# Kernel tuning notes

Hardware: AMD Instinct MI355X
Metric: run time of the kernel (lower is better)

The kernel has to match this reference:

```python
import jax, jax.numpy as jnp
import numpy as np
from jax.scipy.linalg import expm as _expm

B, D = 1024, 128
_SQRT3 = 3.0 ** 0.5
_C1, _C2 = 0.5 - _SQRT3 / 6.0, 0.5 + _SQRT3 / 6.0


def setup_inputs() -> dict:
    key = jax.random.key(0)
    k_t, k_y, k_a, k_w = jax.random.split(key, 4)
    scale = 1.0 / np.sqrt(D)  # keep ||Omega|| moderate so expm is well-conditioned
    return {
        "t0": jax.random.uniform(k_t, (B,), dtype=jnp.float32),
        "h": jnp.float32(0.1),
        "y0": jax.random.normal(k_y, (B, D), dtype=jnp.float32),
        "A0": jax.random.normal(k_a, (B, D, D), dtype=jnp.float32) * scale,
        "W": jax.random.normal(k_w, (B, D, D), dtype=jnp.float32) * scale,
    }


def reference(t0, h, y0, A0, W):
    # A(t) = A0 + t * W evaluated at the two Gauss-Legendre nodes
    t1 = t0 + _C1 * h  # (B,)
    t2 = t0 + _C2 * h  # (B,)
    A1 = A0 + t1[:, None, None] * W  # (B, D, D)
    A2 = A0 + t2[:, None, None] * W  # (B, D, D)
    alpha1 = (h * 0.5) * (A1 + A2)
    alpha2 = (h * _SQRT3) * (A2 - A1)
    comm = alpha1 @ alpha2 - alpha2 @ alpha1  # [alpha1, alpha2]
    Omega = alpha1 - comm / 12.0
    U = jax.vmap(_expm)(Omega)  # batched matrix exponential (B, D, D)
    y_next = jnp.einsum("bij,bj->bi", U, y0)  # (B, D)
    return y_next, jnp.stack((A1, A2), axis=0)
```

## Files before the change

### kernel.cpp

```cpp
#include <hip/hip_runtime.h>

#define B_SZ 1024
#define D_SZ 128
#define KTERMS 8
#define RSTRIDE 68

typedef float vfloat4 __attribute__((ext_vector_type(4)));

__device__ inline float bflo(unsigned u) { return __uint_as_float(u << 16); }
__device__ inline float bfhi(unsigned u) { return __uint_as_float(u & 0xffff0000u); }

__device__ inline float dotlds(const unsigned* rq, const float* v) {
    float a0 = 0.f, a1 = 0.f, a2 = 0.f, a3 = 0.f;
#pragma unroll
    for (int j = 0; j < 8; ++j) {
        uint4 qq = *(const uint4*)(rq + 4 * j);
        vfloat4 v0 = *(const vfloat4*)(v + 8 * j);
        vfloat4 v1 = *(const vfloat4*)(v + 8 * j + 4);
        a0 = fmaf(bflo(qq.x), v0.x, a0);
        a1 = fmaf(bfhi(qq.x), v0.y, a1);
        a2 = fmaf(bflo(qq.y), v0.z, a2);
        a3 = fmaf(bfhi(qq.y), v0.w, a3);
        a0 = fmaf(bflo(qq.z), v1.x, a0);
        a1 = fmaf(bfhi(qq.z), v1.y, a1);
        a2 = fmaf(bflo(qq.w), v1.z, a2);
        a3 = fmaf(bfhi(qq.w), v1.w, a3);
    }
    return (a0 + a1) + (a2 + a3);
}

__global__ void __launch_bounds__(512, 4)
magnus_kernel(const float* __restrict__ t0p, const float* __restrict__ hp,
              const float* __restrict__ y0, const float* __restrict__ A0,
              const float* __restrict__ W, float* __restrict__ out)
{
    __shared__ __align__(16) unsigned sA[D_SZ * RSTRIDE];
    __shared__ __align__(16) unsigned sW[D_SZ * RSTRIDE];
    __shared__ __align__(16) float sv[D_SZ];
    __shared__ __align__(16) float su1[D_SZ];
    __shared__ __align__(16) float su2[D_SZ];
    __shared__ __align__(16) float su3[D_SZ];
    __shared__ __align__(16) float su4[D_SZ];

    const int b = blockIdx.x;
    const int tid = threadIdx.x;
    const float h = hp[0];
    const float tb = t0p[b];
    const float SQ3_6 = 0.28867513459481287f;
    const float t1 = tb + (0.5f - SQ3_6) * h;
    const float t2 = tb + (0.5f + SQ3_6) * h;

    const size_t moff = (size_t)b * (D_SZ * D_SZ);
    const float4* A0v = (const float4*)(A0 + moff);
    const float4* Wv  = (const float4*)(W + moff);
    vfloat4* o1 = (vfloat4*)(out + (size_t)B_SZ * D_SZ + moff);
    vfloat4* o2 = (vfloat4*)(out + (size_t)B_SZ * D_SZ
                                 + (size_t)B_SZ * D_SZ * D_SZ + moff);

#pragma unroll 8
    for (int it = 0; it < 8; ++it) {
        int i = it * 512 + tid;
        float4 a = A0v[i];
        float4 w = Wv[i];
        vfloat4 p1, p2;
        p1.x = fmaf(t1, w.x, a.x); p1.y = fmaf(t1, w.y, a.y);
        p1.z = fmaf(t1, w.z, a.z); p1.w = fmaf(t1, w.w, a.w);
        p2.x = fmaf(t2, w.x, a.x); p2.y = fmaf(t2, w.y, a.y);
        p2.z = fmaf(t2, w.z, a.z); p2.w = fmaf(t2, w.w, a.w);
        __builtin_nontemporal_store(p1, o1 + i);
        __builtin_nontemporal_store(p2, o2 + i);

        unsigned pa0, pa1, pw0, pw1;
        asm("v_cvt_pk_bf16_f32 %0, %1, %2" : "=v"(pa0) : "v"(a.x), "v"(a.y));
        asm("v_cvt_pk_bf16_f32 %0, %1, %2" : "=v"(pa1) : "v"(a.z), "v"(a.w));
        asm("v_cvt_pk_bf16_f32 %0, %1, %2" : "=v"(pw0) : "v"(w.x), "v"(w.y));
        asm("v_cvt_pk_bf16_f32 %0, %1, %2" : "=v"(pw1) : "v"(w.z), "v"(w.w));
        int r = i >> 5;
        int p = (2 * i) & 63;
        *(uint2*)(&sA[r * RSTRIDE + p]) = make_uint2(pa0, pa1);
        *(uint2*)(&sW[r * RSTRIDE + p]) = make_uint2(pw0, pw1);
    }

    const int grp  = tid >> 8;
    const int t8   = tid & 255;
    const int half = (t8 >> 5) & 1;
    const int row  = (t8 & 31) + ((t8 >> 6) << 5);
    const unsigned* rq = (grp ? sW : sA) + row * RSTRIDE + half * 32;

    float yacc = 0.0f;
    if (tid < D_SZ) {
        float v = y0[(size_t)b * D_SZ + tid];
        sv[tid] = v;
        yacc = v;
    }
    __syncthreads();

    const float hs = h * (tb + 0.5f * h);
    const float c3 = h * h * h * (1.0f / 12.0f);

#pragma unroll
    for (int k = 1; k <= KTERMS; ++k) {
        float a = dotlds(rq, sv + half * 64);
        a += __shfl_xor(a, 32);
        if (!half) { if (grp == 0) su1[row] = a; else su2[row] = a; }
        __syncthreads();
        const float* vb = grp ? su1 : su2;
        float c = dotlds(rq, vb + half * 64);
        c += __shfl_xor(c, 32);
        if (!half) { if (grp == 0) su3[row] = c; else su4[row] = c; }
        __syncthreads();
        if (tid < D_SZ) {
            float wn = h * su1[tid] + hs * su2[tid] - c3 * (su3[tid] - su4[tid]);
            wn *= (1.0f / (float)k);
            yacc += wn;
            sv[tid] = wn;
        }
        __syncthreads();
    }

    if (tid < D_SZ) {
        out[(size_t)b * D_SZ + tid] = yacc;
    }
}

extern "C" void kernel_launch(void* const* d_in, const int* in_sizes, int n_in,
                              void* d_out, int out_size, void* d_ws, size_t ws_size,
                              hipStream_t stream) {
    const float* t0 = (const float*)d_in[0];
    const float* h  = (const float*)d_in[1];
    const float* y0 = (const float*)d_in[2];
    const float* A0 = (const float*)d_in[3];
    const float* W  = (const float*)d_in[4];
    float* out = (float*)d_out;
    magnus_kernel<<<B_SZ, 512, 0, stream>>>(t0, h, y0, A0, W, out);
}
```

Measured before the change: 257.2 us.

## Process two batches per block and prefetch next matrices into registers

```diff
diff --git a/kernel.cpp b/kernel.cpp
--- a/kernel.cpp
+++ b/kernel.cpp
@@ -4,6 +4,7 @@
 #define D_SZ 128
 #define KTERMS 8
 #define RSTRIDE 68
+#define NBATCH 2
 
 typedef float vfloat4 __attribute__((ext_vector_type(4)));
 
@@ -42,44 +43,9 @@
     __shared__ __align__(16) float su3[D_SZ];
     __shared__ __align__(16) float su4[D_SZ];
 
-    const int b = blockIdx.x;
     const int tid = threadIdx.x;
     const float h = hp[0];
-    const float tb = t0p[b];
     const float SQ3_6 = 0.28867513459481287f;
-    const float t1 = tb + (0.5f - SQ3_6) * h;
-    const float t2 = tb + (0.5f + SQ3_6) * h;
-
-    const size_t moff = (size_t)b * (D_SZ * D_SZ);
-    const float4* A0v = (const float4*)(A0 + moff);
-    const float4* Wv  = (const float4*)(W + moff);
-    vfloat4* o1 = (vfloat4*)(out + (size_t)B_SZ * D_SZ + moff);
-    vfloat4* o2 = (vfloat4*)(out + (size_t)B_SZ * D_SZ
-                                 + (size_t)B_SZ * D_SZ * D_SZ + moff);
-
-#pragma unroll 8
-    for (int it = 0; it < 8; ++it) {
-        int i = it * 512 + tid;
-        float4 a = A0v[i];
-        float4 w = Wv[i];
-        vfloat4 p1, p2;
-        p1.x = fmaf(t1, w.x, a.x); p1.y = fmaf(t1, w.y, a.y);
-        p1.z = fmaf(t1, w.z, a.z); p1.w = fmaf(t1, w.w, a.w);
-        p2.x = fmaf(t2, w.x, a.x); p2.y = fmaf(t2, w.y, a.y);
-        p2.z = fmaf(t2, w.z, a.z); p2.w = fmaf(t2, w.w, a.w);
-        __builtin_nontemporal_store(p1, o1 + i);
-        __builtin_nontemporal_store(p2, o2 + i);
-
-        unsigned pa0, pa1, pw0, pw1;
-        asm("v_cvt_pk_bf16_f32 %0, %1, %2" : "=v"(pa0) : "v"(a.x), "v"(a.y));
-        asm("v_cvt_pk_bf16_f32 %0, %1, %2" : "=v"(pa1) : "v"(a.z), "v"(a.w));
-        asm("v_cvt_pk_bf16_f32 %0, %1, %2" : "=v"(pw0) : "v"(w.x), "v"(w.y));
-        asm("v_cvt_pk_bf16_f32 %0, %1, %2" : "=v"(pw1) : "v"(w.z), "v"(w.w));
-        int r = i >> 5;
-        int p = (2 * i) & 63;
-        *(uint2*)(&sA[r * RSTRIDE + p]) = make_uint2(pa0, pa1);
-        *(uint2*)(&sW[r * RSTRIDE + p]) = make_uint2(pw0, pw1);
-    }
 
     const int grp  = tid >> 8;
     const int t8   = tid & 255;
@@ -87,39 +53,102 @@
     const int row  = (t8 & 31) + ((t8 >> 6) << 5);
     const unsigned* rq = (grp ? sW : sA) + row * RSTRIDE + half * 32;
 
-    float yacc = 0.0f;
-    if (tid < D_SZ) {
-        float v = y0[(size_t)b * D_SZ + tid];
-        sv[tid] = v;
-        yacc = v;
+    int b = blockIdx.x * NBATCH;
+
+    vfloat4 ra[8], rw[8];
+    {
+        const vfloat4* A0n = (const vfloat4*)(A0 + (size_t)b * (D_SZ * D_SZ));
+        const vfloat4* Wn  = (const vfloat4*)(W  + (size_t)b * (D_SZ * D_SZ));
+#pragma unroll
+        for (int it = 0; it < 8; ++it) {
+            int i = it * 512 + tid;
+            ra[it] = A0n[i];
+            rw[it] = Wn[i];
+        }
     }
-    __syncthreads();
 
-    const float hs = h * (tb + 0.5f * h);
-    const float c3 = h * h * h * (1.0f / 12.0f);
+    for (int g = 0; g < NBATCH; ++g, ++b) {
+        const float tb = t0p[b];
+        const float t1 = tb + (0.5f - SQ3_6) * h;
+        const float t2 = tb + (0.5f + SQ3_6) * h;
+        const size_t moff = (size_t)b * (D_SZ * D_SZ);
+        vfloat4* o1 = (vfloat4*)(out + (size_t)B_SZ * D_SZ + moff);
+        vfloat4* o2 = (vfloat4*)(out + (size_t)B_SZ * D_SZ
+                                     + (size_t)B_SZ * D_SZ * D_SZ + moff);
 
 #pragma unroll
-    for (int k = 1; k <= KTERMS; ++k) {
-        float a = dotlds(rq, sv + half * 64);
-        a += __shfl_xor(a, 32);
-        if (!half) { if (grp == 0) su1[row] = a; else su2[row] = a; }
+        for (int it = 0; it < 8; ++it) {
+            int i = it * 512 + tid;
+            vfloat4 a = ra[it], w = rw[it];
+            vfloat4 p1, p2;
+            p1.x = fmaf(t1, w.x, a.x); p1.y = fmaf(t1, w.y, a.y);
+            p1.z = fmaf(t1, w.z, a.z); p1.w = fmaf(t1, w.w, a.w);
+            p2.x = fmaf(t2, w.x, a.x); p2.y = fmaf(t2, w.y, a.y);
+            p2.z = fmaf(t2, w.z, a.z); p2.w = fmaf(t2, w.w, a.w);
+            __builtin_nontemporal_store(p1, o1 + i);
+            __builtin_nontemporal_store(p2, o2 + i);
+
+            unsigned pa0, pa1, pw0, pw1;
+            asm("v_cvt_pk_bf16_f32 %0, %1, %2" : "=v"(pa0) : "v"(a.x), "v"(a.y));
+            asm("v_cvt_pk_bf16_f32 %0, %1, %2" : "=v"(pa1) : "v"(a.z), "v"(a.w));
+            asm("v_cvt_pk_bf16_f32 %0, %1, %2" : "=v"(pw0) : "v"(w.x), "v"(w.y));
+            asm("v_cvt_pk_bf16_f32 %0, %1, %2" : "=v"(pw1) : "v"(w.z), "v"(w.w));
+            int r = i >> 5;
+            int p = (2 * i) & 63;
+            *(uint2*)(&sA[r * RSTRIDE + p]) = make_uint2(pa0, pa1);
+            *(uint2*)(&sW[r * RSTRIDE + p]) = make_uint2(pw0, pw1);
+        }
+
+        float yacc = 0.0f;
+        if (tid < D_SZ) {
+            float v = y0[(size_t)b * D_SZ + tid];
+            sv[tid] = v;
+            yacc = v;
+        }
+
+        if (g + 1 < NBATCH) {
+            const vfloat4* A0n = (const vfloat4*)(A0 + moff + D_SZ * D_SZ);
+            const vfloat4* Wn  = (const vfloat4*)(W  + moff + D_SZ * D_SZ);
+#pragma unroll
+            for (int it = 0; it < 8; ++it) {
+                int i = it * 512 + tid;
+                ra[it] = A0n[i];
+                rw[it] = Wn[i];
+            }
+#pragma unroll
+            for (int it = 0; it < 8; ++it) {
+                asm volatile("" : "+v"(ra[it]));
+                asm volatile("" : "+v"(rw[it]));
+            }
+        }
+
         __syncthreads();
-        const float* vb = grp ? su1 : su2;
-        float c = dotlds(rq, vb + half * 64);
-        c += __shfl_xor(c, 32);
-        if (!half) { if (grp == 0) su3[row] = c; else su4[row] = c; }
-        __syncthreads();
+
+        const float hs = h * (tb + 0.5f * h);
+        const float c3 = h * h * h * (1.0f / 12.0f);
+#pragma unroll
+        for (int k = 1; k <= KTERMS; ++k) {
+            float a = dotlds(rq, sv + half * 64);
+            a += __shfl_xor(a, 32);
+            if (!half) { if (grp == 0) su1[row] = a; else su2[row] = a; }
+            __syncthreads();
+            const float* vb = grp ? su1 : su2;
+            float c = dotlds(rq, vb + half * 64);
+            c += __shfl_xor(c, 32);
+            if (!half) { if (grp == 0) su3[row] = c; else su4[row] = c; }
+            __syncthreads();
+            if (tid < D_SZ) {
+                float wn = h * su1[tid] + hs * su2[tid] - c3 * (su3[tid] - su4[tid]);
+                wn *= (1.0f / (float)k);
+                yacc += wn;
+                sv[tid] = wn;
+            }
+            __syncthreads();
+        }
+
         if (tid < D_SZ) {
-            float wn = h * su1[tid] + hs * su2[tid] - c3 * (su3[tid] - su4[tid]);
-            wn *= (1.0f / (float)k);
-            yacc += wn;
-            sv[tid] = wn;
+            out[(size_t)b * D_SZ + tid] = yacc;
         }
-        __syncthreads();
-    }
-
-    if (tid < D_SZ) {
-        out[(size_t)b * D_SZ + tid] = yacc;
     }
 }
 
@@ -132,5 +161,5 @@
     const float* A0 = (const float*)d_in[3];
     const float* W  = (const float*)d_in[4];
     float* out = (float*)d_out;
-    magnus_kernel<<<B_SZ, 512, 0, stream>>>(t0, h, y0, A0, W, out);
+    magnus_kernel<<<B_SZ / NBATCH, 512, 0, stream>>>(t0, h, y0, A0, W, out);
 }
```

After: 269.5 us. 4.8% more time.

## Keep bf16 A0/W rows in registers instead of LDS and cut Taylor terms to 7

Applied to the files above, without the earlier changes.

```diff
diff --git a/kernel.cpp b/kernel.cpp
--- a/kernel.cpp
+++ b/kernel.cpp
@@ -2,29 +2,23 @@
 
 #define B_SZ 1024
 #define D_SZ 128
-#define KTERMS 8
-#define RSTRIDE 68
+#define KTERMS 7
+#define QPAD 36
 
 typedef float vfloat4 __attribute__((ext_vector_type(4)));
 
 __device__ inline float bflo(unsigned u) { return __uint_as_float(u << 16); }
 __device__ inline float bfhi(unsigned u) { return __uint_as_float(u & 0xffff0000u); }
 
-__device__ inline float dotlds(const unsigned* rq, const float* v) {
+__device__ inline float dot32(const unsigned* rq, const float* v) {
     float a0 = 0.f, a1 = 0.f, a2 = 0.f, a3 = 0.f;
 #pragma unroll
     for (int j = 0; j < 8; ++j) {
-        uint4 qq = *(const uint4*)(rq + 4 * j);
-        vfloat4 v0 = *(const vfloat4*)(v + 8 * j);
-        vfloat4 v1 = *(const vfloat4*)(v + 8 * j + 4);
-        a0 = fmaf(bflo(qq.x), v0.x, a0);
-        a1 = fmaf(bfhi(qq.x), v0.y, a1);
-        a2 = fmaf(bflo(qq.y), v0.z, a2);
-        a3 = fmaf(bfhi(qq.y), v0.w, a3);
-        a0 = fmaf(bflo(qq.z), v1.x, a0);
-        a1 = fmaf(bfhi(qq.z), v1.y, a1);
-        a2 = fmaf(bflo(qq.w), v1.z, a2);
-        a3 = fmaf(bfhi(qq.w), v1.w, a3);
+        vfloat4 vv = *(const vfloat4*)(v + 4 * j);
+        a0 = fmaf(bflo(rq[2 * j]),     vv.x, a0);
+        a1 = fmaf(bfhi(rq[2 * j]),     vv.y, a1);
+        a2 = fmaf(bflo(rq[2 * j + 1]), vv.z, a2);
+        a3 = fmaf(bfhi(rq[2 * j + 1]), vv.w, a3);
     }
     return (a0 + a1) + (a2 + a3);
 }
@@ -34,86 +28,85 @@
               const float* __restrict__ y0, const float* __restrict__ A0,
               const float* __restrict__ W, float* __restrict__ out)
 {
-    __shared__ __align__(16) unsigned sA[D_SZ * RSTRIDE];
-    __shared__ __align__(16) unsigned sW[D_SZ * RSTRIDE];
-    __shared__ __align__(16) float sv[D_SZ];
-    __shared__ __align__(16) float su1[D_SZ];
-    __shared__ __align__(16) float su2[D_SZ];
-    __shared__ __align__(16) float su3[D_SZ];
-    __shared__ __align__(16) float su4[D_SZ];
+    __shared__ __align__(16) float svr [4 * QPAD];
+    __shared__ __align__(16) float su1r[4 * QPAD];
+    __shared__ __align__(16) float su2r[4 * QPAD];
+    __shared__ __align__(16) float su3r[4 * QPAD];
+    __shared__ __align__(16) float su4r[4 * QPAD];
 
-    const int b = blockIdx.x;
+    const int b   = blockIdx.x;
     const int tid = threadIdx.x;
-    const float h = hp[0];
+    const int row = tid >> 2;
+    const int q   = tid & 3;
+    const float h  = hp[0];
     const float tb = t0p[b];
     const float SQ3_6 = 0.28867513459481287f;
     const float t1 = tb + (0.5f - SQ3_6) * h;
     const float t2 = tb + (0.5f + SQ3_6) * h;
 
     const size_t moff = (size_t)b * (D_SZ * D_SZ);
-    const float4* A0v = (const float4*)(A0 + moff);
-    const float4* Wv  = (const float4*)(W + moff);
-    vfloat4* o1 = (vfloat4*)(out + (size_t)B_SZ * D_SZ + moff);
-    vfloat4* o2 = (vfloat4*)(out + (size_t)B_SZ * D_SZ
-                                 + (size_t)B_SZ * D_SZ * D_SZ + moff);
+    const int fbase = row * 32 + q * 8;
+    const float4* Ap = (const float4*)(A0 + moff) + fbase;
+    const float4* Wp = (const float4*)(W + moff) + fbase;
+    float4* o1 = (float4*)(out + (size_t)B_SZ * D_SZ + moff) + fbase;
+    float4* o2 = (float4*)(out + (size_t)B_SZ * D_SZ
+                               + (size_t)B_SZ * D_SZ * D_SZ + moff) + fbase;
 
-#pragma unroll 8
+    unsigned ra[16], rw[16];
+#pragma unroll
     for (int it = 0; it < 8; ++it) {
-        int i = it * 512 + tid;
-        float4 a = A0v[i];
-        float4 w = Wv[i];
-        vfloat4 p1, p2;
+        float4 a = Ap[it];
+        float4 w = Wp[it];
+        float4 p1, p2;
         p1.x = fmaf(t1, w.x, a.x); p1.y = fmaf(t1, w.y, a.y);
         p1.z = fmaf(t1, w.z, a.z); p1.w = fmaf(t1, w.w, a.w);
         p2.x = fmaf(t2, w.x, a.x); p2.y = fmaf(t2, w.y, a.y);
         p2.z = fmaf(t2, w.z, a.z); p2.w = fmaf(t2, w.w, a.w);
-        __builtin_nontemporal_store(p1, o1 + i);
-        __builtin_nontemporal_store(p2, o2 + i);
-
-        unsigned pa0, pa1, pw0, pw1;
-        asm("v_cvt_pk_bf16_f32 %0, %1, %2" : "=v"(pa0) : "v"(a.x), "v"(a.y));
-        asm("v_cvt_pk_bf16_f32 %0, %1, %2" : "=v"(pa1) : "v"(a.z), "v"(a.w));
-        asm("v_cvt_pk_bf16_f32 %0, %1, %2" : "=v"(pw0) : "v"(w.x), "v"(w.y));
-        asm("v_cvt_pk_bf16_f32 %0, %1, %2" : "=v"(pw1) : "v"(w.z), "v"(w.w));
-        int r = i >> 5;
-        int p = (2 * i) & 63;
-        *(uint2*)(&sA[r * RSTRIDE + p]) = make_uint2(pa0, pa1);
-        *(uint2*)(&sW[r * RSTRIDE + p]) = make_uint2(pw0, pw1);
+        o1[it] = p1;
+        o2[it] = p2;
+        asm("v_cvt_pk_bf16_f32 %0, %1, %2" : "=v"(ra[2*it])   : "v"(a.x), "v"(a.y));
+        asm("v_cvt_pk_bf16_f32 %0, %1, %2" : "=v"(ra[2*it+1]) : "v"(a.z), "v"(a.w));
+        asm("v_cvt_pk_bf16_f32 %0, %1, %2" : "=v"(rw[2*it])   : "v"(w.x), "v"(w.y));
+        asm("v_cvt_pk_bf16_f32 %0, %1, %2" : "=v"(rw[2*it+1]) : "v"(w.z), "v"(w.w));
     }
-
-    const int grp  = tid >> 8;
-    const int t8   = tid & 255;
-    const int half = (t8 >> 5) & 1;
-    const int row  = (t8 & 31) + ((t8 >> 6) << 5);
-    const unsigned* rq = (grp ? sW : sA) + row * RSTRIDE + half * 32;
 
     float yacc = 0.0f;
     if (tid < D_SZ) {
         float v = y0[(size_t)b * D_SZ + tid];
-        sv[tid] = v;
+        svr[(tid >> 5) * QPAD + (tid & 31)] = v;
         yacc = v;
     }
     __syncthreads();
 
     const float hs = h * (tb + 0.5f * h);
     const float c3 = h * h * h * (1.0f / 12.0f);
+    const int uflat = (row >> 5) * QPAD + (row & 31);
 
 #pragma unroll
     for (int k = 1; k <= KTERMS; ++k) {
-        float a = dotlds(rq, sv + half * 64);
-        a += __shfl_xor(a, 32);
-        if (!half) { if (grp == 0) su1[row] = a; else su2[row] = a; }
+        {
+            const float* vq = svr + q * QPAD;
+            float pa = dot32(ra, vq);
+            float pw = dot32(rw, vq);
+            pa += __shfl_xor(pa, 1); pa += __shfl_xor(pa, 2);
+            pw += __shfl_xor(pw, 1); pw += __shfl_xor(pw, 2);
+            if (q == 0) { su1r[uflat] = pa; su2r[uflat] = pw; }
+        }
         __syncthreads();
-        const float* vb = grp ? su1 : su2;
-        float c = dotlds(rq, vb + half * 64);
-        c += __shfl_xor(c, 32);
-        if (!half) { if (grp == 0) su3[row] = c; else su4[row] = c; }
+        {
+            float pb = dot32(ra, su2r + q * QPAD);
+            float pc = dot32(rw, su1r + q * QPAD);
+            pb += __shfl_xor(pb, 1); pb += __shfl_xor(pb, 2);
+            pc += __shfl_xor(pc, 1); pc += __shfl_xor(pc, 2);
+            if (q == 0) { su3r[uflat] = pb; su4r[uflat] = pc; }
+        }
         __syncthreads();
         if (tid < D_SZ) {
-            float wn = h * su1[tid] + hs * su2[tid] - c3 * (su3[tid] - su4[tid]);
+            int f = (tid >> 5) * QPAD + (tid & 31);
+            float wn = h * su1r[f] + hs * su2r[f] - c3 * (su3r[f] - su4r[f]);
             wn *= (1.0f / (float)k);
             yacc += wn;
-            sv[tid] = wn;
+            svr[f] = wn;
         }
         __syncthreads();
     }
```

Measured after the change: 277.5 us. 7.9% more time.
